# Kernel optimization log

Measured on AMD Instinct MI355X. Metric: run time of the kernel, lower is better.

## Reference

```python
import jax, jax.numpy as jnp
import numpy as np

P = 45007
VEC = 4            # default_vec in the triton kernel
BK = 32            # BLOCK_SIZE_K
BN = 32            # BLOCK_SIZE_N
REDN = 2           # reduction factor
IN_FEATURES = 4096
OUT_FEATURES = 4096
RED_IN = ((IN_FEATURES // REDN + BK - 1) // BK) * BK  # 2048


def build_full_idx(random_numbers, K, N, red_in, bk, bn, redn, vec):
    """Vectorized port of SSL.get_idx: flat indices into weight.flatten() for the
    expanded (K, N) weight (i.e. full_weight^T)."""
    R0 = random_numbers[0].astype(jnp.int32)
    R1 = random_numbers[1].astype(jnp.int32)
    R2 = random_numbers[2].astype(jnp.int32)
    R3 = random_numbers[3].astype(jnp.int32)
    ni = K // bk   # number of K blocks
    nj = N // bn   # number of N blocks
    i = jnp.arange(ni, dtype=jnp.int32)
    j = jnp.arange(nj, dtype=jnp.int32)
    it = i // redn                 # [ni]
    itin = i % redn                # [ni]
    h = R3 + R2 * j[None, :] + R1 * (it[:, None] + 1)   # [ni, nj]
    h1 = R0 * (itin + 1)                                 # [ni]
    offset = bk - ((h + h1[:, None]) * vec) % bk         # [ni, nj]
    locs = (offset[:, :, None] + jnp.arange(bk, dtype=jnp.int32)) % bk  # [ni, nj, bk]
    # row index into the compressed weight's reduced-K axis
    row_red = it[:, None, None] * bk + locs              # [ni, nj, bk]
    # reorder so k = i*bk + kk is the leading axis: (ni, bk, nj) -> (K, nj)
    row_red = jnp.transpose(row_red, (0, 2, 1)).reshape(K, nj)
    row_full = jnp.repeat(row_red, bn, axis=1)           # [K, N]
    n_idx = jnp.arange(N, dtype=jnp.int32)[None, :]
    return n_idx * red_in + row_full                     # flat index into weight.flatten()


def setup_inputs() -> dict:
    key = jax.random.key(0)
    k1, k2, k3 = jax.random.split(key, 3)
    x = jax.random.normal(k1, (4, 2048, IN_FEATURES), dtype=jnp.float32)
    # xavier_uniform over (out_features, red_in_features)
    bound_w = float(np.sqrt(6.0 / (OUT_FEATURES + RED_IN)))
    weight = jax.random.uniform(k2, (OUT_FEATURES, RED_IN), dtype=jnp.float32,
                                minval=-bound_w, maxval=bound_w)
    bound_b = 1.0 / float(np.sqrt(IN_FEATURES))
    bias = jax.random.uniform(k3, (OUT_FEATURES,), dtype=jnp.float32,
                              minval=-bound_b, maxval=bound_b)
    # random_numbers = cat([P], 3 ints in [0, P)); fixed representative values
    random_numbers = jnp.array([P, 12345, 6789, 23456], dtype=jnp.int32)
    return {"x": x, "weight": weight, "bias": bias, "random_numbers": random_numbers}


def reference(x, weight, bias, random_numbers):
    K = x.shape[-1]
    N = weight.shape[0]
    full_idx = build_full_idx(random_numbers, K, N, RED_IN, BK, BN, REDN, VEC)  # [K, N]
    w_full = weight.reshape(-1)[full_idx]            # [K, N] = expanded weight^T
    x2 = x.reshape(-1, K)                            # [M, K]
    y = x2 @ w_full + bias[None, :]                  # [M, N]
    return y.reshape(*x.shape[:-1], N)
```

## Files before the change

### kernel.cpp

```cpp
#include <hip/hip_runtime.h>

typedef __bf16 bf16x8 __attribute__((ext_vector_type(8)));
typedef float  f32x4  __attribute__((ext_vector_type(4)));
typedef unsigned short ushort8 __attribute__((ext_vector_type(8)));

#define KDIM  4096
#define NDIM  4096
#define REDIN 2048

static __device__ __forceinline__ unsigned short f2bf(float f) {
    return __builtin_bit_cast(unsigned short, (__bf16)f);
}

typedef __attribute__((address_space(3))) void       lds_void;
typedef const __attribute__((address_space(1))) void gbl_cvoid;

static __device__ __forceinline__ void gload16(const void* g, void* l) {
    __builtin_amdgcn_global_load_lds((gbl_cvoid*)g, (lds_void*)l, 16, 0, 0);
}

__global__ void cvt_x(const float* __restrict__ x, unsigned short* __restrict__ xb,
                      long n8) {
    long idx = (long)blockIdx.x * blockDim.x + threadIdx.x;
    long stride = (long)gridDim.x * blockDim.x;
    for (long i = idx; i < n8; i += stride) {
        const float4 a = ((const float4*)x)[2 * i];
        const float4 b = ((const float4*)x)[2 * i + 1];
        ushort8 s;
        s[0] = f2bf(a.x); s[1] = f2bf(a.y); s[2] = f2bf(a.z); s[3] = f2bf(a.w);
        s[4] = f2bf(b.x); s[5] = f2bf(b.y); s[6] = f2bf(b.z); s[7] = f2bf(b.w);
        ((ushort8*)xb)[i] = s;
    }
}

__global__ void expand_w(const float* __restrict__ w, unsigned short* __restrict__ wx,
                         const int* __restrict__ rn) {
    const int R0 = rn[0], R1 = rn[1], R2 = rn[2], R3 = rn[3];
    const long total = (long)NDIM * (KDIM / 8);
    long idx = (long)blockIdx.x * blockDim.x + threadIdx.x;
    long stride = (long)gridDim.x * blockDim.x;
    for (long t = idx; t < total; t += stride) {
        const int kp = (int)(t & (KDIM / 8 - 1));
        const int n  = (int)(t >> 9);
        const int k0 = kp * 8;
        const int i  = k0 >> 5;
        const int kk0 = k0 & 31;
        const int it = i >> 1;
        const int h  = R3 + R2 * (n >> 5) + R1 * (it + 1) + R0 * ((i & 1) + 1);
        const int off = 32 - ((h << 2) & 31);
        const float* src = w + (long)n * REDIN + it * 32;
        ushort8 s;
#pragma unroll
        for (int q = 0; q < 8; ++q)
            s[q] = f2bf(src[(kk0 + q + off) & 31]);
        ((ushort8*)wx)[t] = s;
    }
}


#define STAGE_H(MAT, T, HALF)                                               \
  {                                                                         \
    char* _d = (char*)lds##MAT + ((((T) & 1) * 2 + (HALF)) * 16384) + tid * 16; \
    const unsigned short* _s = src##MAT + (size_t)((HALF) * 128) * KDIM + (size_t)(T) * 64; \
    gload16(_s, _d);                                                        \
    gload16(_s + (size_t)64 * KDIM, _d + 8192);                             \
  }

#define READ_A(PA, MH)                                                      \
  _Pragma("unroll")                                                         \
  for (int _kk = 0; _kk < 2; ++_kk)                                         \
    _Pragma("unroll")                                                       \
    for (int _mf = 0; _mf < 4; ++_mf)                                       \
      a_[_kk][_mf] = *(const bf16x8*)((PA) + (MH) * 8192 + _mf * 2048 + (roff ^ (_kk << 6)));

#define READ_B(PB, NH)                                                      \
  _Pragma("unroll")                                                         \
  for (int _kk = 0; _kk < 2; ++_kk)                                         \
    _Pragma("unroll")                                                       \
    for (int _nf = 0; _nf < 2; ++_nf)                                       \
      b_##NH[_kk][_nf] = *(const bf16x8*)((PB) + (NH) * 4096 + _nf * 2048 + (roff ^ (_kk << 6)));

#define MFMA_Q(MH, NH)                                                      \
  __builtin_amdgcn_s_setprio(1);                                            \
  _Pragma("unroll")                                                         \
  for (int _kk = 0; _kk < 2; ++_kk)                                         \
    _Pragma("unroll")                                                       \
    for (int _mf = 0; _mf < 4; ++_mf)                                       \
      _Pragma("unroll")                                                     \
      for (int _nf = 0; _nf < 2; ++_nf)                                     \
        acc[(MH) * 4 + _mf][(NH) * 2 + _nf] = __builtin_amdgcn_mfma_f32_16x16x32_bf16( \
            a_[_kk][_mf], b_##NH[_kk][_nf], acc[(MH) * 4 + _mf][(NH) * 2 + _nf], 0, 0, 0); \
  __builtin_amdgcn_s_setprio(0);

#define SB __builtin_amdgcn_sched_barrier(0)
#define BAR __builtin_amdgcn_s_barrier()

#define GROUP(U, BUF, STG, VMSTR)                                           \
  {                                                                         \
    const char* paA = ldsAc + ((BUF) * 2 + wr) * 16384;                     \
    const char* pbB = ldsBc + ((BUF) * 2 + bh) * 16384 + bhw;               \
                                                                    \
    READ_A(paA, 0)                                                          \
    READ_B(pbB, 0)                                                          \
    if ((STG) >= 1) STAGE_H(A, (U) + 1, 0);                                 \
    asm volatile("s_waitcnt lgkmcnt(8)" ::: "memory");                      \
    SB; BAR;                                                                \
    asm volatile("s_waitcnt lgkmcnt(0)" ::: "memory");                      \
    SB;                                                                     \
    MFMA_Q(0, 0)                                                            \
    SB;                                                                     \
                                                                    \
    READ_B(pbB, 1)                                                          \
    if ((STG) >= 1) STAGE_H(A, (U) + 1, 1);                                 \
    SB; BAR;                                                                \
    asm volatile("s_waitcnt lgkmcnt(0)" ::: "memory");                      \
    SB;                                                                     \
    MFMA_Q(0, 1)                                                            \
    SB;                                                                     \
                                                                    \
    READ_A(paA, 1)                                                          \
    if ((STG) >= 2) STAGE_H(B, (U) + 2, 0);                                 \
    SB; BAR;                                                                \
    asm volatile("s_waitcnt lgkmcnt(0)" ::: "memory");                      \
    SB;                                                                     \
    MFMA_Q(1, 1)                                                            \
    SB;                                                                     \
                                                                    \
    if ((STG) >= 2) STAGE_H(B, (U) + 2, 1);                                 \
    SB;                                                                     \
    MFMA_Q(1, 0)                                                            \
    asm volatile("s_waitcnt vmcnt(" VMSTR ")" ::: "memory");                \
    SB; BAR; SB;                                                            \
  }

__global__ __launch_bounds__(512, 2)
void gemm_bt256(const unsigned short* __restrict__ A,
                const unsigned short* __restrict__ B,
                const float* __restrict__ bias,
                float* __restrict__ out, int M)
{
    __shared__ __align__(16) unsigned short ldsA[2 * 2 * 8192];
    __shared__ __align__(16) unsigned short ldsB[2 * 2 * 8192];
    const char* ldsAc = (const char*)ldsA;
    const char* ldsBc = (const char*)ldsB;

    const int nwg = gridDim.x;
    const int bid = blockIdx.x;
    int swzb = bid;
    if ((nwg & 7) == 0) {
        const int cpx = nwg >> 3;
        swzb = (bid & 7) * cpx + (bid >> 3);
    }
    const int ntn = NDIM / 256;
    const int n0 = (swzb % ntn) * 256;
    const int m0 = (swzb / ntn) * 256;

    const int tid  = threadIdx.x;
    const int lane = tid & 63;
    const int wid  = tid >> 6;
    const int wr   = wid >> 2;
    const int wc   = wid & 3;
    const int bh   = wc >> 1;
    const int bhw  = (wc & 1) * 8192;
    const int lrow = lane & 15;
    const int g    = lane >> 4;
    const int x7   = lrow & 7;

    const int roff = lrow * 128 + (((g ^ x7) & 7) << 4);

    const int srow = tid >> 3;
    const int sslot = (tid & 7) ^ (srow & 7);
    const unsigned short* srcA = A + (size_t)(m0 + srow) * KDIM + 8 * sslot;
    const unsigned short* srcB = B + (size_t)(n0 + srow) * KDIM + 8 * sslot;

    f32x4 acc[8][4];
#pragma unroll
    for (int m = 0; m < 8; ++m)
#pragma unroll
        for (int n = 0; n < 4; ++n)
            acc[m][n] = (f32x4)(0.0f);

    bf16x8 a_[2][4], b_0[2][2], b_1[2][2];

    STAGE_H(A, 0, 0);
    STAGE_H(A, 0, 1);
    STAGE_H(B, 0, 0);
    STAGE_H(B, 0, 1);
    STAGE_H(B, 1, 0);
    STAGE_H(B, 1, 1);
    asm volatile("s_waitcnt vmcnt(4)" ::: "memory");
    SB; BAR; SB;

    for (int u = 0; u < 62; u += 2) {
        GROUP(u,     0, 2, "4");
        GROUP(u + 1, 1, 2, "4");
    }
    GROUP(62, 0, 1, "0");
    GROUP(63, 1, 0, "0");

#pragma unroll
    for (int nh = 0; nh < 2; ++nh)
#pragma unroll
        for (int nf = 0; nf < 2; ++nf) {
            const int col = n0 + wc * 64 + nh * 32 + nf * 16 + lrow;
            const float bv = bias[col];
#pragma unroll
            for (int mh = 0; mh < 2; ++mh)
#pragma unroll
                for (int mf = 0; mf < 4; ++mf) {
                    const size_t rbase = (size_t)(m0 + wr * 128 + mh * 64 + mf * 16 + (lane >> 4) * 4);
#pragma unroll
                    for (int e = 0; e < 4; ++e)
                        out[(rbase + e) * NDIM + col] = acc[mh * 4 + mf][nh * 2 + nf][e] + bv;
                }
        }
}

__global__ __launch_bounds__(256, 2)
void ssl_gemm_fused(const float* __restrict__ x, const float* __restrict__ w,
                    const float* __restrict__ bias, const int* __restrict__ rn,
                    float* __restrict__ out)
{
    __shared__ __align__(16) unsigned short As[128][40];
    __shared__ __align__(16) unsigned short Bs[128][40];

    const int R0 = rn[0], R1 = rn[1], R2 = rn[2], R3 = rn[3];
    const int tid = threadIdx.x;
    const int n0 = blockIdx.x * 128;
    const int m0 = blockIdx.y * 128;
    const int srow = tid >> 3;
    const int scol = (tid & 7) * 4;
    const int lane = tid & 63;
    const int wid  = tid >> 6;
    const int wr   = wid >> 1;
    const int wc   = wid & 1;
    const int lrow = lane & 15;
    const int lk   = (lane >> 4) * 8;

    f32x4 acc[4][4];
#pragma unroll
    for (int m = 0; m < 4; ++m)
#pragma unroll
        for (int n = 0; n < 4; ++n)
            acc[m][n] = (f32x4)(0.0f);

    for (int i = 0; i < KDIM / 32; ++i) {
        const int it   = i >> 1;
        const int k0   = i * 32;
#pragma unroll
        for (int p = 0; p < 4; ++p) {
            const int row = p * 32 + srow;
            const float4 v = *(const float4*)(x + (size_t)(m0 + row) * KDIM + k0 + scol);
            ushort4 s;
            s.x = f2bf(v.x); s.y = f2bf(v.y); s.z = f2bf(v.z); s.w = f2bf(v.w);
            *(ushort4*)&As[row][scol] = s;
        }
        const int hbase = R3 + R1 * (it + 1) + R0 * ((i & 1) + 1);
#pragma unroll
        for (int p = 0; p < 4; ++p) {
            const int nl = p * 32 + srow;
            const int j  = (n0 + nl) >> 5;
            const int off = 32 - (((hbase + R2 * j) << 2) & 31);
            const float4 v = *(const float4*)(w + (size_t)(n0 + nl) * REDIN + it * 32 + scol);
            Bs[nl][(scol + 0 - off) & 31] = f2bf(v.x);
            Bs[nl][(scol + 1 - off) & 31] = f2bf(v.y);
            Bs[nl][(scol + 2 - off) & 31] = f2bf(v.z);
            Bs[nl][(scol + 3 - off) & 31] = f2bf(v.w);
        }
        __syncthreads();

        bf16x8 af[4], bfr[4];
#pragma unroll
        for (int m = 0; m < 4; ++m)
            af[m] = *(const bf16x8*)&As[wr * 64 + m * 16 + lrow][lk];
#pragma unroll
        for (int n = 0; n < 4; ++n)
            bfr[n] = *(const bf16x8*)&Bs[wc * 64 + n * 16 + lrow][lk];
#pragma unroll
        for (int m = 0; m < 4; ++m)
#pragma unroll
            for (int n = 0; n < 4; ++n)
                acc[m][n] = __builtin_amdgcn_mfma_f32_16x16x32_bf16(af[m], bfr[n], acc[m][n], 0, 0, 0);
        __syncthreads();
    }

#pragma unroll
    for (int n = 0; n < 4; ++n) {
        const int col = n0 + wc * 64 + n * 16 + lrow;
        const float bv = bias[col];
#pragma unroll
        for (int m = 0; m < 4; ++m) {
            const int rbase = m0 + wr * 64 + m * 16 + (lane >> 4) * 4;
#pragma unroll
            for (int e = 0; e < 4; ++e)
                out[(size_t)(rbase + e) * NDIM + col] = acc[m][n][e] + bv;
        }
    }
}

extern "C" void kernel_launch(void* const* d_in, const int* in_sizes, int n_in,
                              void* d_out, int out_size, void* d_ws, size_t ws_size,
                              hipStream_t stream) {
    const float* x    = (const float*)d_in[0];
    const float* wgt  = (const float*)d_in[1];
    const float* bias = (const float*)d_in[2];
    const int*   rn   = (const int*)d_in[3];
    float* out = (float*)d_out;

    const int M = in_sizes[0] / KDIM;
    const size_t need = ((size_t)M * KDIM + (size_t)NDIM * KDIM) * sizeof(unsigned short);

    if (ws_size >= need && (M % 256) == 0) {
        unsigned short* xb = (unsigned short*)d_ws;
        unsigned short* wx = xb + (size_t)M * KDIM;

        cvt_x<<<2048, 256, 0, stream>>>(x, xb, (long)M * KDIM / 8);
        expand_w<<<2048, 256, 0, stream>>>(wgt, wx, rn);

        const int nwg = (NDIM / 256) * (M / 256);
        gemm_bt256<<<nwg, 512, 0, stream>>>(xb, wx, bias, out, M);
    } else {
        dim3 grid(NDIM / 128, M / 128);
        ssl_gemm_fused<<<grid, dim3(256), 0, stream>>>(x, wgt, bias, rn, out);
    }
}
```

Baseline: 273.5 us.

## Triple-buffer A tiles in LDS and prefetch two K-steps ahead

The GEMM main loop now keeps three LDS buffers for A and two for B, and issues both A and B global-to-LDS loads two iterations ahead. Before, A was prefetched only one step ahead. The loop is unrolled by six so the buffer indices rotate at compile time, and the vmcnt waits are loosened to allow more loads in flight. This is meant to hide more global-load latency, at the cost of extra LDS: about 160KB total against 128KB before. That may conflict with the launch bound of two workgroups per CU and lower occupancy.

```diff
diff --git a/kernel.cpp b/kernel.cpp
--- a/kernel.cpp
+++ b/kernel.cpp
@@ -58,10 +58,18 @@
 }
 
 
-#define STAGE_H(MAT, T, HALF)                                               \
+#define STAGE_A(T, BUFI, HALF)                                              \
   {                                                                         \
-    char* _d = (char*)lds##MAT + ((((T) & 1) * 2 + (HALF)) * 16384) + tid * 16; \
-    const unsigned short* _s = src##MAT + (size_t)((HALF) * 128) * KDIM + (size_t)(T) * 64; \
+    char* _d = (char*)ldsA + (BUFI) * 32768 + (HALF) * 16384 + tid * 16;    \
+    const unsigned short* _s = srcA + (size_t)((HALF) * 128) * KDIM + (size_t)(T) * 64; \
+    gload16(_s, _d);                                                        \
+    gload16(_s + (size_t)64 * KDIM, _d + 8192);                             \
+  }
+
+#define STAGE_B(T, BUFI, HALF)                                              \
+  {                                                                         \
+    char* _d = (char*)ldsB + (BUFI) * 32768 + (HALF) * 16384 + tid * 16;    \
+    const unsigned short* _s = srcB + (size_t)((HALF) * 128) * KDIM + (size_t)(T) * 64; \
     gload16(_s, _d);                                                        \
     gload16(_s + (size_t)64 * KDIM, _d + 8192);                             \
   }
@@ -95,14 +103,14 @@
 #define SB __builtin_amdgcn_sched_barrier(0)
 #define BAR __builtin_amdgcn_s_barrier()
 
-#define GROUP(U, BUF, STG, VMSTR)                                           \
+#define GROUP(U, AB, ASB, BB, STG, VMSTR)                                   \
   {                                                                         \
-    const char* paA = ldsAc + ((BUF) * 2 + wr) * 16384;                     \
-    const char* pbB = ldsBc + ((BUF) * 2 + bh) * 16384 + bhw;               \
+    const char* paA = ldsAc + (AB) * 32768 + wr * 16384;                    \
+    const char* pbB = ldsBc + (BB) * 32768 + bh * 16384 + bhw;              \
                                                                     \
     READ_A(paA, 0)                                                          \
     READ_B(pbB, 0)                                                          \
-    if ((STG) >= 1) STAGE_H(A, (U) + 1, 0);                                 \
+    if ((STG) >= 2) STAGE_A((U) + 2, (ASB), 0);                             \
     asm volatile("s_waitcnt lgkmcnt(8)" ::: "memory");                      \
     SB; BAR;                                                                \
     asm volatile("s_waitcnt lgkmcnt(0)" ::: "memory");                      \
@@ -111,7 +119,7 @@
     SB;                                                                     \
                                                                     \
     READ_B(pbB, 1)                                                          \
-    if ((STG) >= 1) STAGE_H(A, (U) + 1, 1);                                 \
+    if ((STG) >= 2) STAGE_A((U) + 2, (ASB), 1);                             \
     SB; BAR;                                                                \
     asm volatile("s_waitcnt lgkmcnt(0)" ::: "memory");                      \
     SB;                                                                     \
@@ -119,14 +127,15 @@
     SB;                                                                     \
                                                                     \
     READ_A(paA, 1)                                                          \
-    if ((STG) >= 2) STAGE_H(B, (U) + 2, 0);                                 \
     SB; BAR;                                                                \
     asm volatile("s_waitcnt lgkmcnt(0)" ::: "memory");                      \
     SB;                                                                     \
+    if ((STG) >= 2) STAGE_B((U) + 2, (BB), 0);                              \
+    SB;                                                                     \
     MFMA_Q(1, 1)                                                            \
     SB;                                                                     \
                                                                     \
-    if ((STG) >= 2) STAGE_H(B, (U) + 2, 1);                                 \
+    if ((STG) >= 2) STAGE_B((U) + 2, (BB), 1);                              \
     SB;                                                                     \
     MFMA_Q(1, 0)                                                            \
     asm volatile("s_waitcnt vmcnt(" VMSTR ")" ::: "memory");                \
@@ -139,8 +148,8 @@
                 const float* __restrict__ bias,
                 float* __restrict__ out, int M)
 {
-    __shared__ __align__(16) unsigned short ldsA[2 * 2 * 8192];
-    __shared__ __align__(16) unsigned short ldsB[2 * 2 * 8192];
+    __shared__ __align__(16) unsigned short ldsA[3 * 16384];
+    __shared__ __align__(16) unsigned short ldsB[2 * 16384];
     const char* ldsAc = (const char*)ldsA;
     const char* ldsBc = (const char*)ldsB;
 
@@ -182,21 +191,25 @@
 
     bf16x8 a_[2][4], b_0[2][2], b_1[2][2];
 
-    STAGE_H(A, 0, 0);
-    STAGE_H(A, 0, 1);
-    STAGE_H(B, 0, 0);
-    STAGE_H(B, 0, 1);
-    STAGE_H(B, 1, 0);
-    STAGE_H(B, 1, 1);
-    asm volatile("s_waitcnt vmcnt(4)" ::: "memory");
+    STAGE_A(0, 0, 0); STAGE_A(0, 0, 1);
+    STAGE_B(0, 0, 0); STAGE_B(0, 0, 1);
+    STAGE_A(1, 1, 0); STAGE_A(1, 1, 1);
+    STAGE_B(1, 1, 0); STAGE_B(1, 1, 1);
+    asm volatile("s_waitcnt vmcnt(8)" ::: "memory");
     SB; BAR; SB;
 
-    for (int u = 0; u < 62; u += 2) {
-        GROUP(u,     0, 2, "4");
-        GROUP(u + 1, 1, 2, "4");
-    }
-    GROUP(62, 0, 1, "0");
-    GROUP(63, 1, 0, "0");
+    for (int u = 0; u < 60; u += 6) {
+        GROUP(u + 0, 0, 2, 0, 2, "8");
+        GROUP(u + 1, 1, 0, 1, 2, "8");
+        GROUP(u + 2, 2, 1, 0, 2, "8");
+        GROUP(u + 3, 0, 2, 1, 2, "8");
+        GROUP(u + 4, 1, 0, 0, 2, "8");
+        GROUP(u + 5, 2, 1, 1, 2, "8");
+    }
+    GROUP(60, 0, 2, 0, 2, "8");
+    GROUP(61, 1, 0, 1, 2, "8");
+    GROUP(62, 2, 1, 0, 0, "0");
+    GROUP(63, 0, 2, 1, 0, "0");
 
 #pragma unroll
     for (int nh = 0; nh < 2; ++nh)
```

Result: slower. 279.3 us (+2.1%).
